# Performance work log

Measured on AMD Instinct MI355X. Metric: run time of the kernel, lower is better.

Reference implementation:

```python
import jax, jax.numpy as jnp
import numpy as np


def setup_inputs() -> dict:
    key = jax.random.key(0)
    ks = jax.random.split(key, 13)
    B, D, H, O = 4096, 2048, 3, 1  # batch, input_dim, hidden layer count, output_dim
    f32 = jnp.float32
    scale = 1.0 / np.sqrt(D)
    return {
        "x": jax.random.normal(ks[0], (B, D), f32),
        "w_mu_h": jax.random.normal(ks[1], (H, D, D), f32) * scale,
        "w_rho_h": jax.random.normal(ks[2], (H, D, D), f32) - 5.0,  # softplus(-5) ~ small std
        "b_mu_h": jax.random.normal(ks[3], (H, D), f32) * scale,
        "b_rho_h": jax.random.normal(ks[4], (H, D), f32) - 5.0,
        "w_mu_o": jax.random.normal(ks[5], (O, D), f32) * scale,
        "w_rho_o": jax.random.normal(ks[6], (O, D), f32) - 5.0,
        "b_mu_o": jax.random.normal(ks[7], (O,), f32) * scale,
        "b_rho_o": jax.random.normal(ks[8], (O,), f32) - 5.0,
        # reparameterization noise (torch.randn_like), passed explicitly for determinism
        "eps_w_h": jax.random.normal(ks[9], (H, D, D), f32),
        "eps_b_h": jax.random.normal(ks[10], (H, D), f32),
        "eps_w_o": jax.random.normal(ks[11], (O, D), f32),
        "eps_b_o": jax.random.normal(ks[12], (O,), f32),
    }


def _vlinear(x, w_mu, w_rho, b_mu, b_rho, eps_w, eps_b):
    # weight = mu + eps * softplus(rho); F.linear(x, W, b) = x @ W.T + b
    w = w_mu + eps_w * jax.nn.softplus(w_rho)
    b = b_mu + eps_b * jax.nn.softplus(b_rho)
    return x @ w.T + b


def reference(x, w_mu_h, w_rho_h, b_mu_h, b_rho_h,
              w_mu_o, w_rho_o, b_mu_o, b_rho_o,
              eps_w_h, eps_b_h, eps_w_o, eps_b_o):
    def step(h, p):
        wm, wr, bm, br, ew, eb = p
        h = jax.nn.relu(_vlinear(h, wm, wr, bm, br, ew, eb))
        return h, None

    h, _ = jax.lax.scan(step, x, (w_mu_h, w_rho_h, b_mu_h, b_rho_h, eps_w_h, eps_b_h))
    return _vlinear(h, w_mu_o, w_rho_o, b_mu_o, b_rho_o, eps_w_o, eps_b_o)
```

## Files before the change

### kernel.cpp

```cpp
#include <hip/hip_runtime.h>

#define BB 4096
#define DD 2048

typedef float f32x4 __attribute__((ext_vector_type(4)));
typedef __bf16 bf16x8 __attribute__((ext_vector_type(8)));

typedef __attribute__((address_space(1))) unsigned int gl_u32;
typedef __attribute__((address_space(3))) unsigned int lds_u32;

#define GLOAD_LDS16(gptr, sptr) \
  __builtin_amdgcn_global_load_lds((gl_u32*)(void*)(gptr), (lds_u32*)(sptr), 16, 0, 0)

__device__ __forceinline__ unsigned short f2bf(float f) {
  unsigned int u = __float_as_uint(f);
  u += 0x7fffu + ((u >> 16) & 1u);
  return (unsigned short)(u >> 16);
}

__device__ __forceinline__ float sp(float x) {
  float t = __expf(-fabsf(x));
  return fmaxf(x, 0.0f) + __logf(1.0f + t);
}

__global__ void prep_kernel(
    const float* __restrict__ x,
    const float* __restrict__ wmuh, const float* __restrict__ wrhoh,
    const float* __restrict__ bmuh, const float* __restrict__ brhoh,
    const float* __restrict__ wmuo, const float* __restrict__ wrhoo,
    const float* __restrict__ bmuo, const float* __restrict__ brhoo,
    const float* __restrict__ epswh, const float* __restrict__ epsbh,
    const float* __restrict__ epswo, const float* __restrict__ epsbo,
    unsigned short* __restrict__ Wh, unsigned short* __restrict__ Xb,
    float* __restrict__ bh, float* __restrict__ wo, float* __restrict__ bo)
{
  const int b = blockIdx.x;
  const int t = threadIdx.x;
  if (b < 3072) {
    long long base = (long long)b * 1024 + t;
    float4 m[4], r[4], e[4];
    #pragma unroll
    for (int j = 0; j < 4; ++j) {
      m[j] = ((const float4*)wmuh)[base + j * 256];
      r[j] = ((const float4*)wrhoh)[base + j * 256];
      e[j] = ((const float4*)epswh)[base + j * 256];
    }
    #pragma unroll
    for (int j = 0; j < 4; ++j) {
      ushort4 o;
      o.x = f2bf(m[j].x + e[j].x * sp(r[j].x));
      o.y = f2bf(m[j].y + e[j].y * sp(r[j].y));
      o.z = f2bf(m[j].z + e[j].z * sp(r[j].z));
      o.w = f2bf(m[j].w + e[j].w * sp(r[j].w));
      ((ushort4*)Wh)[base + j * 256] = o;
    }
    return;
  }
  if (b < 5120) {
    long long base = (long long)(b - 3072) * 1024 + t;
    float4 v[4];
    #pragma unroll
    for (int j = 0; j < 4; ++j) v[j] = ((const float4*)x)[base + j * 256];
    #pragma unroll
    for (int j = 0; j < 4; ++j) {
      ushort4 o;
      o.x = f2bf(v[j].x); o.y = f2bf(v[j].y); o.z = f2bf(v[j].z); o.w = f2bf(v[j].w);
      ((ushort4*)Xb)[base + j * 256] = o;
    }
    return;
  }
  long long i = (long long)(b - 5120) * 256 + t;
  if (i < 1536) {
    float4 m = ((const float4*)bmuh)[i];
    float4 r = ((const float4*)brhoh)[i];
    float4 e = ((const float4*)epsbh)[i];
    float4 o;
    o.x = m.x + e.x * sp(r.x);
    o.y = m.y + e.y * sp(r.y);
    o.z = m.z + e.z * sp(r.z);
    o.w = m.w + e.w * sp(r.w);
    ((float4*)bh)[i] = o;
    return;
  }
  i -= 1536;
  if (i < 512) {
    float4 m = ((const float4*)wmuo)[i];
    float4 r = ((const float4*)wrhoo)[i];
    float4 e = ((const float4*)epswo)[i];
    float4 o;
    o.x = m.x + e.x * sp(r.x);
    o.y = m.y + e.y * sp(r.y);
    o.z = m.z + e.z * sp(r.z);
    o.w = m.w + e.w * sp(r.w);
    ((float4*)wo)[i] = o;
    return;
  }
  i -= 512;
  if (i == 0) {
    bo[0] = bmuo[0] + epsbo[0] * sp(brhoo[0]);
  }
}

__global__ __launch_bounds__(512) void gemm_relu_kernel(
    const unsigned short* __restrict__ A,
    const unsigned short* __restrict__ W,
    const float* __restrict__ bias,
    unsigned short* __restrict__ C,
    int N, int K)
{
  __shared__ unsigned short sA[128 * 64];
  __shared__ unsigned short sB[128 * 64];

  const int t = threadIdx.x;
  const int w = t >> 6;
  const int l = t & 63;
  const int lq = l >> 4;
  const int lr = l & 15;

  const int id = blockIdx.x;
  const int p = id & 7;
  const int i4 = id >> 3;
  const int mt = (p & 3) * 8 + (i4 & 7);
  const int nt = (p >> 2) * 8 + (i4 >> 3);
  const int m0 = mt * 128;
  const int n0 = nt * 128;

  const int mw = (w >> 2) * 64;
  const int nw = (w & 3) * 32;

  f32x4 acc[4][2] = {};

  int srow[2], sgc[2];
  #pragma unroll
  for (int i = 0; i < 2; ++i) {
    int c = i * 512 + t;
    srow[i] = c >> 3;
    sgc[i] = (c & 7) ^ (srow[i] & 7);
  }

  for (int kt = 0; kt < K; kt += 64) {
    #pragma unroll
    for (int i = 0; i < 2; ++i) {
      int c = i * 512 + t;
      const unsigned short* ga = A + (size_t)(m0 + srow[i]) * K + kt + sgc[i] * 8;
      GLOAD_LDS16(ga, &sA[c * 8]);
      const unsigned short* gb = W + (size_t)(n0 + srow[i]) * K + kt + sgc[i] * 8;
      GLOAD_LDS16(gb, &sB[c * 8]);
    }
    __syncthreads();

    #pragma unroll
    for (int s = 0; s < 2; ++s) {
      bf16x8 af[4], bfr[2];
      int g = s * 4 + lq;
      #pragma unroll
      for (int i = 0; i < 4; ++i) {
        int ra = mw + i * 16 + lr;
        af[i] = *(const bf16x8*)&sA[ra * 64 + (g ^ (ra & 7)) * 8];
      }
      #pragma unroll
      for (int j = 0; j < 2; ++j) {
        int rb = nw + j * 16 + lr;
        bfr[j] = *(const bf16x8*)&sB[rb * 64 + (g ^ (rb & 7)) * 8];
      }
      #pragma unroll
      for (int i = 0; i < 4; ++i)
        #pragma unroll
        for (int j = 0; j < 2; ++j)
          acc[i][j] = __builtin_amdgcn_mfma_f32_16x16x32_bf16(af[i], bfr[j], acc[i][j], 0, 0, 0);
    }
    __syncthreads();
  }

  #pragma unroll
  for (int j = 0; j < 2; ++j) {
    int n = n0 + nw + j * 16 + lr;
    float bv = bias[n];
    #pragma unroll
    for (int i = 0; i < 4; ++i) {
      int mbase = m0 + mw + i * 16 + lq * 4;
      #pragma unroll
      for (int r = 0; r < 4; ++r) {
        float v = acc[i][j][r] + bv;
        v = fmaxf(v, 0.0f);
        C[(size_t)(mbase + r) * N + n] = f2bf(v);
      }
    }
  }
}

__global__ void final_kernel(const unsigned short* __restrict__ H,
                             const float* __restrict__ wo,
                             const float* __restrict__ bo,
                             float* __restrict__ out)
{
  const int row = blockIdx.x * 4 + (threadIdx.x >> 6);
  const int l = threadIdx.x & 63;
  const unsigned short* hr = H + (size_t)row * DD;
  float sum = 0.0f;
  #pragma unroll
  for (int s = 0; s < 4; ++s) {
    int k = s * 512 + l * 8;
    uint4 hv = *(const uint4*)&hr[k];
    float4 w0 = *(const float4*)&wo[k];
    float4 w1 = *(const float4*)&wo[k + 4];
    sum += __uint_as_float(hv.x << 16) * w0.x;
    sum += __uint_as_float(hv.x & 0xffff0000u) * w0.y;
    sum += __uint_as_float(hv.y << 16) * w0.z;
    sum += __uint_as_float(hv.y & 0xffff0000u) * w0.w;
    sum += __uint_as_float(hv.z << 16) * w1.x;
    sum += __uint_as_float(hv.z & 0xffff0000u) * w1.y;
    sum += __uint_as_float(hv.w << 16) * w1.z;
    sum += __uint_as_float(hv.w & 0xffff0000u) * w1.w;
  }
  #pragma unroll
  for (int off = 32; off > 0; off >>= 1)
    sum += __shfl_down(sum, off, 64);
  if (l == 0) out[row] = sum + bo[0];
}

extern "C" void kernel_launch(void* const* d_in, const int* in_sizes, int n_in,
                              void* d_out, int out_size, void* d_ws, size_t ws_size,
                              hipStream_t stream) {
  const float* x     = (const float*)d_in[0];
  const float* wmuh  = (const float*)d_in[1];
  const float* wrhoh = (const float*)d_in[2];
  const float* bmuh  = (const float*)d_in[3];
  const float* brhoh = (const float*)d_in[4];
  const float* wmuo  = (const float*)d_in[5];
  const float* wrhoo = (const float*)d_in[6];
  const float* bmuo  = (const float*)d_in[7];
  const float* brhoo = (const float*)d_in[8];
  const float* epswh = (const float*)d_in[9];
  const float* epsbh = (const float*)d_in[10];
  const float* epswo = (const float*)d_in[11];
  const float* epsbo = (const float*)d_in[12];

  char* ws = (char*)d_ws;
  unsigned short* Wh = (unsigned short*)(ws);
  unsigned short* Xb = (unsigned short*)(ws + 25165824);
  unsigned short* Ha = (unsigned short*)(ws + 25165824 + 16777216);
  unsigned short* Hb = (unsigned short*)(ws + 25165824 + 2 * 16777216);
  float* bh = (float*)(ws + 25165824 + 3 * 16777216);
  float* wo = (float*)(ws + 25165824 + 3 * 16777216 + 24576);
  float* bo = (float*)(ws + 25165824 + 3 * 16777216 + 24576 + 8192);

  prep_kernel<<<5129, 256, 0, stream>>>(
      x, wmuh, wrhoh, bmuh, brhoh, wmuo, wrhoo, bmuo, brhoo,
      epswh, epsbh, epswo, epsbo, Wh, Xb, bh, wo, bo);

  const int ggrid = (BB / 128) * (DD / 128);
  gemm_relu_kernel<<<ggrid, 512, 0, stream>>>(Xb, Wh,               bh,          Ha, DD, DD);
  gemm_relu_kernel<<<ggrid, 512, 0, stream>>>(Ha, Wh + 1 * 4194304, bh + DD,     Hb, DD, DD);
  gemm_relu_kernel<<<ggrid, 512, 0, stream>>>(Hb, Wh + 2 * 4194304, bh + 2 * DD, Xb, DD, DD);

  final_kernel<<<BB / 4, 256, 0, stream>>>(Xb, wo, bo, (float*)d_out);
}
```

Measured before the change: 315.9 us.

## Overlap layer 2-3 weight prep with first GEMM in a fused launch

Only layer-1 weights, x and layer-1 bias are prepared in the first kernel. The layer-2/3 weight sampling, remaining biases and output-layer params are handled by extra blocks appended to the first GEMM launch, so the bandwidth-bound softplus/bf16 conversion runs alongside the compute-bound GEMM. It also adds launch_bounds occupancy hints of 4. Correctness relies on later GEMM launches being stream-ordered after the fused launch. The risk is that the prep blocks compete with the GEMM blocks for CUs.

```diff
diff --git a/kernel.cpp b/kernel.cpp
--- a/kernel.cpp
+++ b/kernel.cpp
@@ -23,85 +23,185 @@
   return fmaxf(x, 0.0f) + __logf(1.0f + t);
 }
 
-__global__ void prep_kernel(
+__device__ __forceinline__ void prep_w_vec4(
+    const float* __restrict__ mu, const float* __restrict__ rho,
+    const float* __restrict__ eps, unsigned short* __restrict__ Wh,
+    long long i)
+{
+  float4 m = ((const float4*)mu)[i];
+  float4 r = ((const float4*)rho)[i];
+  float4 e = ((const float4*)eps)[i];
+  ushort4 o;
+  o.x = f2bf(m.x + e.x * sp(r.x));
+  o.y = f2bf(m.y + e.y * sp(r.y));
+  o.z = f2bf(m.z + e.z * sp(r.z));
+  o.w = f2bf(m.w + e.w * sp(r.w));
+  ((ushort4*)Wh)[i] = o;
+}
+
+__device__ __forceinline__ void prep_f32_vec4(
+    const float* __restrict__ mu, const float* __restrict__ rho,
+    const float* __restrict__ eps, float* __restrict__ out, long long i)
+{
+  float4 m = ((const float4*)mu)[i];
+  float4 r = ((const float4*)rho)[i];
+  float4 e = ((const float4*)eps)[i];
+  float4 o;
+  o.x = m.x + e.x * sp(r.x);
+  o.y = m.y + e.y * sp(r.y);
+  o.z = m.z + e.z * sp(r.z);
+  o.w = m.w + e.w * sp(r.w);
+  ((float4*)out)[i] = o;
+}
+
+__global__ __launch_bounds__(512) void prep0_kernel(
     const float* __restrict__ x,
+    const float* __restrict__ wmuh, const float* __restrict__ wrhoh,
+    const float* __restrict__ bmuh, const float* __restrict__ brhoh,
+    const float* __restrict__ epswh, const float* __restrict__ epsbh,
+    unsigned short* __restrict__ Wh, unsigned short* __restrict__ Xb,
+    float* __restrict__ bh)
+{
+  const int b = blockIdx.x;
+  const int t = threadIdx.x;
+  if (b < 512) {
+    long long base = (long long)b * 2048 + t;
+    #pragma unroll
+    for (int j = 0; j < 4; ++j)
+      prep_w_vec4(wmuh, wrhoh, epswh, Wh, base + j * 512);
+    return;
+  }
+  if (b < 1536) {
+    long long base = (long long)(b - 512) * 2048 + t;
+    #pragma unroll
+    for (int j = 0; j < 4; ++j) {
+      float4 v = ((const float4*)x)[base + j * 512];
+      ushort4 o;
+      o.x = f2bf(v.x); o.y = f2bf(v.y); o.z = f2bf(v.z); o.w = f2bf(v.w);
+      ((ushort4*)Xb)[base + j * 512] = o;
+    }
+    return;
+  }
+  prep_f32_vec4(bmuh, brhoh, epsbh, bh, t);
+}
+
+#define NGEMM 512
+
+__global__ __launch_bounds__(512, 4) void gemm_relu_fused_kernel(
+    const unsigned short* __restrict__ A,
+    const unsigned short* __restrict__ W,
+    const float* __restrict__ bias,
+    unsigned short* __restrict__ C,
+    int N, int K, int fuse_prep,
     const float* __restrict__ wmuh, const float* __restrict__ wrhoh,
     const float* __restrict__ bmuh, const float* __restrict__ brhoh,
     const float* __restrict__ wmuo, const float* __restrict__ wrhoo,
     const float* __restrict__ bmuo, const float* __restrict__ brhoo,
     const float* __restrict__ epswh, const float* __restrict__ epsbh,
     const float* __restrict__ epswo, const float* __restrict__ epsbo,
-    unsigned short* __restrict__ Wh, unsigned short* __restrict__ Xb,
-    float* __restrict__ bh, float* __restrict__ wo, float* __restrict__ bo)
-{
-  const int b = blockIdx.x;
+    unsigned short* __restrict__ Wh, float* __restrict__ bh,
+    float* __restrict__ wo, float* __restrict__ bo)
+{
+  __shared__ unsigned short sA[128 * 64];
+  __shared__ unsigned short sB[128 * 64];
+
+  const int id = blockIdx.x;
   const int t = threadIdx.x;
-  if (b < 3072) {
-    long long base = (long long)b * 1024 + t;
-    float4 m[4], r[4], e[4];
-    #pragma unroll
-    for (int j = 0; j < 4; ++j) {
-      m[j] = ((const float4*)wmuh)[base + j * 256];
-      r[j] = ((const float4*)wrhoh)[base + j * 256];
-      e[j] = ((const float4*)epswh)[base + j * 256];
-    }
-    #pragma unroll
-    for (int j = 0; j < 4; ++j) {
-      ushort4 o;
-      o.x = f2bf(m[j].x + e[j].x * sp(r[j].x));
-      o.y = f2bf(m[j].y + e[j].y * sp(r[j].y));
-      o.z = f2bf(m[j].z + e[j].z * sp(r[j].z));
-      o.w = f2bf(m[j].w + e[j].w * sp(r[j].w));
-      ((ushort4*)Wh)[base + j * 256] = o;
-    }
+
+  if (id >= NGEMM) {
+    const int pb = id - NGEMM;
+    if (pb < 1024) {
+      long long base = 1048576LL + (long long)pb * 2048 + t;
+      #pragma unroll
+      for (int j = 0; j < 4; ++j)
+        prep_w_vec4(wmuh, wrhoh, epswh, Wh, base + j * 512);
+      return;
+    }
+    #pragma unroll
+    for (int j = 0; j < 2; ++j)
+      prep_f32_vec4(bmuh, brhoh, epsbh, bh, 512 + j * 512 + t);
+    prep_f32_vec4(wmuo, wrhoo, epswo, wo, t);
+    if (t == 0) bo[0] = bmuo[0] + epsbo[0] * sp(brhoo[0]);
     return;
   }
-  if (b < 5120) {
-    long long base = (long long)(b - 3072) * 1024 + t;
-    float4 v[4];
-    #pragma unroll
-    for (int j = 0; j < 4; ++j) v[j] = ((const float4*)x)[base + j * 256];
-    #pragma unroll
-    for (int j = 0; j < 4; ++j) {
-      ushort4 o;
-      o.x = f2bf(v[j].x); o.y = f2bf(v[j].y); o.z = f2bf(v[j].z); o.w = f2bf(v[j].w);
-      ((ushort4*)Xb)[base + j * 256] = o;
-    }
-    return;
-  }
-  long long i = (long long)(b - 5120) * 256 + t;
-  if (i < 1536) {
-    float4 m = ((const float4*)bmuh)[i];
-    float4 r = ((const float4*)brhoh)[i];
-    float4 e = ((const float4*)epsbh)[i];
-    float4 o;
-    o.x = m.x + e.x * sp(r.x);
-    o.y = m.y + e.y * sp(r.y);
-    o.z = m.z + e.z * sp(r.z);
-    o.w = m.w + e.w * sp(r.w);
-    ((float4*)bh)[i] = o;
-    return;
-  }
-  i -= 1536;
-  if (i < 512) {
-    float4 m = ((const float4*)wmuo)[i];
-    float4 r = ((const float4*)wrhoo)[i];
-    float4 e = ((const float4*)epswo)[i];
-    float4 o;
-    o.x = m.x + e.x * sp(r.x);
-    o.y = m.y + e.y * sp(r.y);
-    o.z = m.z + e.z * sp(r.z);
-    o.w = m.w + e.w * sp(r.w);
-    ((float4*)wo)[i] = o;
-    return;
-  }
-  i -= 512;
-  if (i == 0) {
-    bo[0] = bmuo[0] + epsbo[0] * sp(brhoo[0]);
-  }
-}
-
-__global__ __launch_bounds__(512) void gemm_relu_kernel(
+
+  const int w = t >> 6;
+  const int l = t & 63;
+  const int lq = l >> 4;
+  const int lr = l & 15;
+
+  const int p = id & 7;
+  const int i4 = id >> 3;
+  const int mt = (p & 3) * 8 + (i4 & 7);
+  const int nt = (p >> 2) * 8 + (i4 >> 3);
+  const int m0 = mt * 128;
+  const int n0 = nt * 128;
+
+  const int mw = (w >> 2) * 64;
+  const int nw = (w & 3) * 32;
+
+  f32x4 acc[4][2] = {};
+
+  int srow[2], sgc[2];
+  #pragma unroll
+  for (int i = 0; i < 2; ++i) {
+    int c = i * 512 + t;
+    srow[i] = c >> 3;
+    sgc[i] = (c & 7) ^ (srow[i] & 7);
+  }
+
+  for (int kt = 0; kt < K; kt += 64) {
+    #pragma unroll
+    for (int i = 0; i < 2; ++i) {
+      int c = i * 512 + t;
+      const unsigned short* ga = A + (size_t)(m0 + srow[i]) * K + kt + sgc[i] * 8;
+      GLOAD_LDS16(ga, &sA[c * 8]);
+      const unsigned short* gb = W + (size_t)(n0 + srow[i]) * K + kt + sgc[i] * 8;
+      GLOAD_LDS16(gb, &sB[c * 8]);
+    }
+    __syncthreads();
+
+    #pragma unroll
+    for (int s = 0; s < 2; ++s) {
+      bf16x8 af[4], bfr[2];
+      int g = s * 4 + lq;
+      #pragma unroll
+      for (int i = 0; i < 4; ++i) {
+        int ra = mw + i * 16 + lr;
+        af[i] = *(const bf16x8*)&sA[ra * 64 + (g ^ (ra & 7)) * 8];
+      }
+      #pragma unroll
+      for (int j = 0; j < 2; ++j) {
+        int rb = nw + j * 16 + lr;
+        bfr[j] = *(const bf16x8*)&sB[rb * 64 + (g ^ (rb & 7)) * 8];
+      }
+      #pragma unroll
+      for (int i = 0; i < 4; ++i)
+        #pragma unroll
+        for (int j = 0; j < 2; ++j)
+          acc[i][j] = __builtin_amdgcn_mfma_f32_16x16x32_bf16(af[i], bfr[j], acc[i][j], 0, 0, 0);
+    }
+    __syncthreads();
+  }
+
+  #pragma unroll
+  for (int j = 0; j < 2; ++j) {
+    int n = n0 + nw + j * 16 + lr;
+    float bv = bias[n];
+    #pragma unroll
+    for (int i = 0; i < 4; ++i) {
+      int mbase = m0 + mw + i * 16 + lq * 4;
+      #pragma unroll
+      for (int r = 0; r < 4; ++r) {
+        float v = acc[i][j][r] + bv;
+        v = fmaxf(v, 0.0f);
+        C[(size_t)(mbase + r) * N + n] = f2bf(v);
+      }
+    }
+  }
+}
+
+__global__ __launch_bounds__(512, 4) void gemm_relu_kernel(
     const unsigned short* __restrict__ A,
     const unsigned short* __restrict__ W,
     const float* __restrict__ bias,
@@ -245,14 +345,16 @@
   float* wo = (float*)(ws + 25165824 + 3 * 16777216 + 24576);
   float* bo = (float*)(ws + 25165824 + 3 * 16777216 + 24576 + 8192);
 
-  prep_kernel<<<5129, 256, 0, stream>>>(
-      x, wmuh, wrhoh, bmuh, brhoh, wmuo, wrhoo, bmuo, brhoo,
-      epswh, epsbh, epswo, epsbo, Wh, Xb, bh, wo, bo);
-
-  const int ggrid = (BB / 128) * (DD / 128);
-  gemm_relu_kernel<<<ggrid, 512, 0, stream>>>(Xb, Wh,               bh,          Ha, DD, DD);
-  gemm_relu_kernel<<<ggrid, 512, 0, stream>>>(Ha, Wh + 1 * 4194304, bh + DD,     Hb, DD, DD);
-  gemm_relu_kernel<<<ggrid, 512, 0, stream>>>(Hb, Wh + 2 * 4194304, bh + 2 * DD, Xb, DD, DD);
+  prep0_kernel<<<1537, 512, 0, stream>>>(
+      x, wmuh, wrhoh, bmuh, brhoh, epswh, epsbh, Wh, Xb, bh);
+
+  gemm_relu_fused_kernel<<<NGEMM + 1025, 512, 0, stream>>>(
+      Xb, Wh, bh, Ha, DD, DD, 1,
+      wmuh, wrhoh, bmuh, brhoh, wmuo, wrhoo, bmuo, brhoo,
+      epswh, epsbh, epswo, epsbo, Wh, bh, wo, bo);
+
+  gemm_relu_kernel<<<NGEMM, 512, 0, stream>>>(Ha, Wh + 1 * 4194304, bh + DD,     Hb, DD, DD);
+  gemm_relu_kernel<<<NGEMM, 512, 0, stream>>>(Hb, Wh + 2 * 4194304, bh + 2 * DD, Xb, DD, DD);
 
   final_kernel<<<BB / 4, 256, 0, stream>>>(Xb, wo, bo, (float*)d_out);
 }
```

Result: faster. 304.8 us (-3.5%).
